# Performance work log

Measured on AMD Instinct MI355X. Metric: run time of the kernel, lower is better.

The kernel has to match this reference:

```python
import jax, jax.numpy as jnp
import numpy as np

# dims
N, E, Z, C, NB = 8192, 131072, 10, 128, 8
R_MAX, P_CUT, AVG_NEIGH = 5.0, 5, 16.0
SH_DIM, N_L, N_LAYERS, MLP_H = 16, 4, 2, 16
# which l each of the 16 sh components belongs to
L_OF_M = jnp.array([0, 1, 1, 1, 2, 2, 2, 2, 2, 3, 3, 3, 3, 3, 3, 3])


def spherical_harmonics(u):
    """Real spherical harmonics up to l=3, e3nn 'component' normalization. u: [E,3] unit vectors."""
    x, y, z = u[:, 0], u[:, 1], u[:, 2]
    x2, y2, z2 = x * x, y * y, z * z
    s3, s5, s15 = np.sqrt(3.0), np.sqrt(5.0), np.sqrt(15.0)
    a33, a32, a31, a30 = 0.25 * np.sqrt(70.0), np.sqrt(105.0), 0.25 * np.sqrt(42.0), 0.5 * np.sqrt(7.0)
    Y = [jnp.ones_like(x),
         s3 * x, s3 * y, s3 * z,
         s15 * x * y, s15 * y * z, 0.5 * s5 * (3 * z2 - 1.0), s15 * x * z, 0.5 * s15 * (x2 - y2),
         a33 * y * (3 * x2 - y2), a32 * x * y * z, a31 * y * (5 * z2 - 1.0),
         a30 * z * (5 * z2 - 3.0), a31 * x * (5 * z2 - 1.0), 0.5 * a32 * z * (x2 - y2),
         a33 * x * (x2 - 3 * y2)]
    return jnp.stack(Y, axis=-1)  # [E,16]


def radial_embedding(r):
    """Bessel radial basis with smooth polynomial cutoff (p=5). r: [E] edge lengths."""
    x = r / R_MAX
    p = float(P_CUT)
    cut = (1.0 - 0.5 * (p + 1.0) * (p + 2.0) * x ** P_CUT
           + p * (p + 2.0) * x ** (P_CUT + 1) - 0.5 * p * (p + 1.0) * x ** (P_CUT + 2))
    cut = jnp.where(x < 1.0, cut, 0.0)
    n = jnp.arange(1, NB + 1, dtype=r.dtype)
    bessel = np.sqrt(2.0 / R_MAX) * jnp.sin(n[None, :] * jnp.pi * x[:, None]) / r[:, None]
    return bessel * cut[:, None]  # [E,8]


def _forward(positions, node_attrs, shifts, W_embed, W_up, R_w1, R_w2, R_w3,
             W_out, w_sc, w_prod, W_plin, w_ro0, ro_w1, ro_w2, edge_index):
    sender, receiver = edge_index[0], edge_index[1]
    vec = positions[receiver] - positions[sender] + shifts          # [E,3]
    lengths = jnp.linalg.norm(vec, axis=-1) + 1e-9                  # [E]
    sh = spherical_harmonics(vec / lengths[:, None])                # [E,16]
    edge_feats = radial_embedding(lengths)                          # [E,8]

    # node embedding: scalars into l=0 slot of [N,C,16]
    scalars = node_attrs @ W_embed                                  # [N,C]
    feats = jnp.zeros((N, C, SH_DIM), scalars.dtype).at[:, :, 0].set(scalars)

    outputs = []
    for L in range(N_LAYERS):
        # linear up (channel mixing, per irrep component)
        h = jnp.einsum('ncm,cd->ndm', feats, W_up[L])               # [N,C,16]
        # radial MLP -> per-edge, per-channel, per-l tensor-product weights
        r = jax.nn.silu(edge_feats @ R_w1[L])
        r = jax.nn.silu(r @ R_w2[L])
        w = (r @ R_w3[L]).reshape(E, C, N_L)                        # [E,C,4]
        w_m = jnp.take(w, L_OF_M, axis=2)                           # [E,C,16]
        # channel-wise tensor product: scalar node feat x SH, scatter to receiver
        msg = h[sender, :, 0][:, :, None] * w_m * sh[:, None, :]    # [E,C,16]
        agg = jax.ops.segment_sum(msg, receiver, num_segments=N) / AVG_NEIGH
        m = jnp.einsum('ncm,cd->ndm', agg, W_out[L])                # [N,C,16]
        # element-dependent skip connection
        sc = h * (node_attrs @ w_sc[L])[:, :, None]
        # product basis (correlation 3): element-weighted powers of scalar part
        s = m[:, :, 0]                                              # [N,C]
        coeff = jnp.einsum('nz,zck->nck', node_attrs, w_prod[L])    # [N,C,3]
        powers = jnp.stack([jnp.ones_like(s), s, s * s], axis=-1)   # [N,C,3]
        scale = jnp.sum(coeff * powers, axis=-1)                    # [N,C]
        feats = jnp.einsum('ncm,cd->ndm', m * scale[:, :, None], W_plin[L]) + sc
        if L == 0:
            outputs.append(feats[:, :, 0] @ w_ro0)                  # linear readout [N]
        else:
            outputs.append(jax.nn.silu(feats[:, :, 0] @ ro_w1) @ ro_w2)  # nonlinear readout [N]
    return outputs[0] + outputs[1]


def setup_inputs() -> dict:
    key = jax.random.key(0)
    ks = jax.random.split(key, 16)
    positions = jax.random.normal(ks[0], (N, 3), jnp.float32) * 1.5
    elems = jax.random.randint(ks[1], (N,), 0, Z)
    node_attrs = jax.nn.one_hot(elems, Z, dtype=jnp.float32)
    edge_index = jax.random.randint(ks[2], (2, E), 0, N)
    shifts = jnp.zeros((E, 3), jnp.float32)
    g = lambda k, sh, fan: jax.random.normal(k, sh, jnp.float32) / np.sqrt(fan)
    return {
        'positions': positions, 'node_attrs': node_attrs, 'shifts': shifts,
        'W_embed': g(ks[3], (Z, C), Z),
        'W_up': g(ks[4], (N_LAYERS, C, C), C),
        'R_w1': g(ks[5], (N_LAYERS, NB, 64), NB),
        'R_w2': g(ks[6], (N_LAYERS, 64, 64), 64),
        'R_w3': g(ks[7], (N_LAYERS, 64, C * N_L), 64),
        'W_out': g(ks[8], (N_LAYERS, C, C), C),
        'w_sc': g(ks[9], (N_LAYERS, Z, C), 1),
        'w_prod': g(ks[10], (N_LAYERS, Z, C, 3), 1) * 0.1,
        'W_plin': g(ks[11], (N_LAYERS, C, C), C),
        'w_ro0': g(ks[12], (C,), C),
        'ro_w1': g(ks[13], (C, MLP_H), C),
        'ro_w2': g(ks[14], (MLP_H,), MLP_H),
        'edge_index': edge_index,
    }


def reference(positions, node_attrs, shifts, W_embed, W_up, R_w1, R_w2, R_w3,
              W_out, w_sc, w_prod, W_plin, w_ro0, ro_w1, ro_w2, edge_index):
    return _forward(positions, node_attrs, shifts, W_embed, W_up, R_w1, R_w2, R_w3,
                    W_out, w_sc, w_prod, W_plin, w_ro0, ro_w1, ro_w2, edge_index)
```

## Files before the change

kernel.cpp:

```cpp
#include <hip/hip_runtime.h>
#include <math.h>

constexpr int kN = 8192;
constexpr int kE = 131072;
constexpr int kHalfN = 4096;
constexpr int kWbTiles = 544;
constexpr int kWbRows  = kWbTiles * 128;

typedef short bf16x8 __attribute__((ext_vector_type(8)));
typedef float f32x4 __attribute__((ext_vector_type(4)));
typedef unsigned short ushort_t;
typedef unsigned int uint_t;

__device__ __forceinline__ float silu_f(float x) { return x / (1.f + __expf(-x)); }

__device__ __forceinline__ ushort_t f2b(float f) {
  uint_t x = __float_as_uint(f);
  uint_t r = (x + 0x7fffu + ((x >> 16) & 1u)) >> 16;
  return (ushort_t)r;
}
__device__ __forceinline__ float b2f(ushort_t u) {
  return __uint_as_float(((uint_t)u) << 16);
}

__global__ __launch_bounds__(256) void zero_ints_kernel(int* __restrict__ a, int* __restrict__ b) {
  int i = blockIdx.x * 256 + threadIdx.x;
  if (i < kN) { a[i] = 0; b[i] = 0; }
}

__global__ __launch_bounds__(256) void elem_kernel(const float* __restrict__ attrs, int* __restrict__ elem) {
  int n = blockIdx.x * 256 + threadIdx.x;
  if (n >= kN) return;
  const float* a = attrs + (size_t)n * 10;
  int best = 0; float bv = a[0];
  #pragma unroll
  for (int z = 1; z < 10; ++z) { float v = a[z]; if (v > bv) { bv = v; best = z; } }
  elem[n] = best;
}

__global__ __launch_bounds__(256) void init_feats_kernel(const float* __restrict__ W_embed,
                                                         const int* __restrict__ elem,
                                                         ushort_t* __restrict__ F) {
  int i = blockIdx.x * 256 + threadIdx.x;
  int n = i >> 7, c = i & 127;
  F[(size_t)n * 2048 + c] = f2b(W_embed[(size_t)elem[n] * 128 + c]);
}

__global__ __launch_bounds__(256) void count_kernel(const int* __restrict__ ei, int* __restrict__ counts) {
  int e = blockIdx.x * 256 + threadIdx.x;
  if (e < kE) atomicAdd(&counts[ei[kE + e]], 1);
}

__global__ __launch_bounds__(1024) void scan_kernel(const int* __restrict__ counts, int* __restrict__ offs) {
  __shared__ int tmp[1024];
  int t = threadIdx.x;
  int loc[8]; int s = 0;
  #pragma unroll
  for (int i = 0; i < 8; ++i) { loc[i] = s; s += counts[t*8 + i]; }
  tmp[t] = s;
  __syncthreads();
  for (int d = 1; d < 1024; d <<= 1) {
    int v = (t >= d) ? tmp[t - d] : 0;
    __syncthreads();
    tmp[t] += v;
    __syncthreads();
  }
  int pre = (t == 0) ? 0 : tmp[t - 1];
  #pragma unroll
  for (int i = 0; i < 8; ++i) offs[t*8 + i] = pre + loc[i];
  if (t == 1023) offs[kN] = tmp[1023];
}

__global__ __launch_bounds__(256) void fill_kernel(const int* __restrict__ ei, const int* __restrict__ offs,
                                                   int* __restrict__ cursor, int* __restrict__ eids,
                                                   int* __restrict__ sends) {
  int e = blockIdx.x * 256 + threadIdx.x;
  if (e >= kE) return;
  int s = ei[e];
  int r = ei[kE + e];
  int pos = atomicAdd(&cursor[r], 1);
  eids[offs[r] + pos] = e;
  sends[offs[r] + pos] = s;
}

__global__ __launch_bounds__(256) void geom_kernel(const float* __restrict__ pos,
                                                   const float* __restrict__ shifts,
                                                   const int* __restrict__ ei,
                                                   const int* __restrict__ eids,
                                                   const int* __restrict__ sends,
                                                   float* __restrict__ sh,
                                                   float* __restrict__ rb) {
  int slot = blockIdx.x * 256 + threadIdx.x;
  if (slot >= kE) return;
  int e = eids[slot];
  int s = sends[slot];
  int r = ei[kE + e];
  float vx = pos[r*3+0] - pos[s*3+0] + shifts[(size_t)e*3+0];
  float vy = pos[r*3+1] - pos[s*3+1] + shifts[(size_t)e*3+1];
  float vz = pos[r*3+2] - pos[s*3+2] + shifts[(size_t)e*3+2];
  float len = sqrtf(vx*vx + vy*vy + vz*vz) + 1e-9f;
  float inv = 1.f / len;
  float x = vx*inv, y = vy*inv, z = vz*inv;
  float x2 = x*x, y2 = y*y, z2 = z*z;
  const float s3  = 1.7320508075688772f;
  const float s5  = 2.2360679774997896f;
  const float s15 = 3.8729833462074170f;
  const float a33 = 2.0916500663351889f;
  const float a32 = 10.246950765959598f;
  const float a31 = 1.6201851746019651f;
  const float a30 = 1.3228756555322954f;
  float4* shp = (float4*)(sh + (size_t)slot * 16);
  shp[0] = make_float4(1.f, s3*x, s3*y, s3*z);
  shp[1] = make_float4(s15*x*y, s15*y*z, 0.5f*s5*(3.f*z2 - 1.f), s15*x*z);
  shp[2] = make_float4(0.5f*s15*(x2 - y2), a33*y*(3.f*x2 - y2), a32*x*y*z, a31*y*(5.f*z2 - 1.f));
  shp[3] = make_float4(a30*z*(5.f*z2 - 3.f), a31*x*(5.f*z2 - 1.f), 0.5f*a32*z*(x2 - y2), a33*x*(x2 - 3.f*y2));
  float xr = len * 0.2f;
  float cut = 0.f;
  if (xr < 1.f) {
    float x5 = xr*xr*xr*xr*xr;
    cut = 1.f - 21.f*x5 + 35.f*x5*xr - 15.f*x5*xr*xr;
  }
  float pref = 0.63245553203367587f * cut * inv;
  const float PI = 3.14159265358979323846f;
  float theta = PI * xr;
  float sn, cs;
  __sincosf(theta, &sn, &cs);
  float twoc = 2.f * cs;
  float b[8];
  float s_prev = 0.f, s_cur = sn;
  b[0] = pref * s_cur;
  #pragma unroll
  for (int k = 1; k < 8; ++k) {
    float s_next = twoc * s_cur - s_prev;
    s_prev = s_cur; s_cur = s_next;
    b[k] = pref * s_cur;
  }
  float4* rbp = (float4*)(rb + (size_t)slot * 8);
  rbp[0] = make_float4(b[0], b[1], b[2], b[3]);
  rbp[1] = make_float4(b[4], b[5], b[6], b[7]);
}

__global__ __launch_bounds__(256) void radial_kernel(const float* __restrict__ rb,
                                                     const float* __restrict__ W1,
                                                     const float* __restrict__ W2,
                                                     ushort_t* __restrict__ r2) {
  __shared__ float rbs[128][8];
  __shared__ float W1s[8*64];
  __shared__ ushort_t B2s[64][72];
  __shared__ ushort_t r1s[128][72];
  const int tid = threadIdx.x;
  const size_t ebase = (size_t)blockIdx.x * 128;
  {
    int r = tid >> 1, q = tid & 1;
    *(float4*)&rbs[r][q*4] = *(const float4*)&rb[(ebase + r)*8 + q*4];
  }
  for (int i = tid; i < 512; i += 256) W1s[i] = W1[i];
  for (int i = tid; i < 4096; i += 256) {
    int k = i >> 6, col = i & 63;
    B2s[col][k] = f2b(W2[i]);
  }
  __syncthreads();
  {
    int col = tid & 63;
    int r0 = (tid >> 6) * 32;
    #pragma unroll 4
    for (int rr = 0; rr < 32; ++rr) {
      int row = r0 + rr;
      float v = 0.f;
      #pragma unroll
      for (int i = 0; i < 8; ++i) v = fmaf(rbs[row][i], W1s[i*64 + col], v);
      r1s[row][col] = f2b(silu_f(v));
    }
  }
  __syncthreads();
  const int lane = tid & 63, wv = tid >> 6;
  const int wr = wv * 32;
  const int fr = lane & 15, kg = (lane >> 4) * 8;
  f32x4 acc[2][4] = {};
  #pragma unroll
  for (int ks = 0; ks < 2; ++ks) {
    const int k0 = ks*32 + kg;
    bf16x8 af[2], bfr[4];
    #pragma unroll
    for (int i = 0; i < 2; ++i) af[i] = *(const bf16x8*)&r1s[wr + i*16 + fr][k0];
    #pragma unroll
    for (int j = 0; j < 4; ++j) bfr[j] = *(const bf16x8*)&B2s[j*16 + fr][k0];
    #pragma unroll
    for (int i = 0; i < 2; ++i)
      #pragma unroll
      for (int j = 0; j < 4; ++j)
        acc[i][j] = __builtin_amdgcn_mfma_f32_16x16x32_bf16(af[i], bfr[j], acc[i][j], 0, 0, 0);
  }
  __syncthreads();
  const int dcol = lane & 15, drow4 = (lane >> 4) * 4;
  #pragma unroll
  for (int i = 0; i < 2; ++i)
    #pragma unroll
    for (int j = 0; j < 4; ++j)
      #pragma unroll
      for (int r = 0; r < 4; ++r) {
        int row = wr + i*16 + drow4 + r;
        int col = j*16 + dcol;
        r1s[row][col] = f2b(silu_f(acc[i][j][r]));
      }
  __syncthreads();
  for (int idx = tid * 8; idx < 128*64; idx += 256*8) {
    int r = idx >> 6, k = idx & 63;
    *(int4*)&r2[(ebase + r)*64 + k] = *(const int4*)&r1s[r][k];
  }
}

__global__ __launch_bounds__(256) void transpose_w_kernel(const float* __restrict__ W, ushort_t* __restrict__ WT) {
  int i = blockIdx.x * 256 + threadIdx.x;
  int d = i >> 7, c = i & 127;
  WT[i] = f2b(W[c*128 + d]);
}

__global__ __launch_bounds__(256) void transpose_r3_kernel(const float* __restrict__ R3, ushort_t* __restrict__ R3T) {
  int i = blockIdx.x * 256 + threadIdx.x;
  int t = i >> 6, j = i & 63;
  int c = t & 127, l = t >> 7;
  R3T[i] = f2b(R3[j*512 + c*4 + l]);
}

template<bool SCALED, bool EPI, bool L0>
__global__ __launch_bounds__(256) void mgemm_kernel(
    const ushort_t* __restrict__ A, size_t aStride,
    const ushort_t* __restrict__ BT,
    ushort_t* __restrict__ O, size_t oStride,
    const float* __restrict__ scaleBuf,
    const ushort_t* __restrict__ Hbuf,
    const float* __restrict__ wscL,
    const int* __restrict__ elem)
{
  __shared__ ushort_t As[128][136];
  __shared__ ushort_t Bs[128][136];
  const int tid = threadIdx.x;
  const size_t rowbase = (size_t)blockIdx.x * 128;

  for (int idx = tid * 8; idx < 128 * 128; idx += 256 * 8) {
    int r = idx >> 7, k = idx & 127;
    *(int4*)&Bs[r][k] = *(const int4*)&BT[(size_t)r * 128 + k];
  }
  for (int idx = tid * 8; idx < 128 * 128; idx += 256 * 8) {
    int r = idx >> 7, k = idx & 127;
    size_t grow = rowbase + r;
    const ushort_t* ap = A + grow * aStride + k;
    if (SCALED) {
      const float* sp = scaleBuf + (grow >> 4) * 128 + k;
      uint_t u[4];
      #pragma unroll
      for (int q = 0; q < 4; ++q) {
        ushort_t lo = f2b(b2f(ap[2*q])   * sp[2*q]);
        ushort_t hi = f2b(b2f(ap[2*q+1]) * sp[2*q+1]);
        u[q] = (uint_t)lo | ((uint_t)hi << 16);
      }
      *(int4*)&As[r][k] = make_int4((int)u[0], (int)u[1], (int)u[2], (int)u[3]);
    } else {
      *(int4*)&As[r][k] = *(const int4*)ap;
    }
  }
  __syncthreads();

  const int lane = tid & 63, wv = tid >> 6;
  const int wr = (wv >> 1) * 64, wc = (wv & 1) * 64;
  const int fr = lane & 15;
  const int kg = (lane >> 4) * 8;
  f32x4 acc[4][4] = {};
  #pragma unroll
  for (int ks = 0; ks < 4; ++ks) {
    const int k0 = ks * 32 + kg;
    bf16x8 af[4], bfr[4];
    #pragma unroll
    for (int i = 0; i < 4; ++i) af[i]  = *(const bf16x8*)&As[wr + i*16 + fr][k0];
    #pragma unroll
    for (int j = 0; j < 4; ++j) bfr[j] = *(const bf16x8*)&Bs[wc + j*16 + fr][k0];
    #pragma unroll
    for (int i = 0; i < 4; ++i)
      #pragma unroll
      for (int j = 0; j < 4; ++j)
        acc[i][j] = __builtin_amdgcn_mfma_f32_16x16x32_bf16(af[i], bfr[j], acc[i][j], 0, 0, 0);
  }

  const int dcol = lane & 15, drow4 = (lane >> 4) * 4;
  #pragma unroll
  for (int i = 0; i < 4; ++i) {
    #pragma unroll
    for (int j = 0; j < 4; ++j) {
      int col = wc + j*16 + dcol;
      #pragma unroll
      for (int r = 0; r < 4; ++r) {
        int row = wr + i*16 + drow4 + r;
        size_t grow = rowbase + row;
        float v = acc[i][j][r];
        if (EPI) {
          if (!L0 || ((grow & 15) == 0)) {
            int ee = elem[grow >> 4];
            v += b2f(Hbuf[grow * 128 + col]) * wscL[(size_t)ee * 128 + col];
          }
        }
        O[grow * oStride + col] = f2b(v);
      }
    }
  }
}

__global__ __launch_bounds__(256) void wgemm_kernel(
    const ushort_t* __restrict__ r2,
    const int* __restrict__ offs, int nb0,
    const ushort_t* __restrict__ R3T, ushort_t* __restrict__ wb)
{
  __shared__ ushort_t As[128][72];
  __shared__ ushort_t Bs[128][72];
  const int tid = threadIdx.x;
  const int rowbase = blockIdx.x * 128;
  const int colbase = blockIdx.y * 128;
  const int halfStart = offs[nb0];

  for (int idx = tid * 8; idx < 128 * 64; idx += 256 * 8) {
    int r = idx >> 6, k = idx & 63;
    *(int4*)&Bs[r][k] = *(const int4*)&R3T[(size_t)(colbase + r) * 64 + k];
  }
  for (int idx = tid * 8; idx < 128 * 64; idx += 256 * 8) {
    int r = idx >> 6, k = idx & 63;
    int slot = halfStart + rowbase + r;
    if (slot > kE - 1) slot = kE - 1;
    *(int4*)&As[r][k] = *(const int4*)&r2[(size_t)slot * 64 + k];
  }
  __syncthreads();

  const int lane = tid & 63, wv = tid >> 6;
  const int wr = (wv >> 1) * 64, wc = (wv & 1) * 64;
  const int fr = lane & 15;
  const int kg = (lane >> 4) * 8;
  f32x4 acc[4][4] = {};
  #pragma unroll
  for (int ks = 0; ks < 2; ++ks) {
    const int k0 = ks * 32 + kg;
    bf16x8 af[4], bfr[4];
    #pragma unroll
    for (int i = 0; i < 4; ++i) af[i]  = *(const bf16x8*)&As[wr + i*16 + fr][k0];
    #pragma unroll
    for (int j = 0; j < 4; ++j) bfr[j] = *(const bf16x8*)&Bs[wc + j*16 + fr][k0];
    #pragma unroll
    for (int i = 0; i < 4; ++i)
      #pragma unroll
      for (int j = 0; j < 4; ++j)
        acc[i][j] = __builtin_amdgcn_mfma_f32_16x16x32_bf16(af[i], bfr[j], acc[i][j], 0, 0, 0);
  }

  const int dcol = lane & 15, drow4 = (lane >> 4) * 4;
  #pragma unroll
  for (int i = 0; i < 4; ++i) {
    #pragma unroll
    for (int j = 0; j < 4; ++j) {
      int col = colbase + wc + j*16 + dcol;
      #pragma unroll
      for (int r = 0; r < 4; ++r) {
        int row = rowbase + wr + i*16 + drow4 + r;
        wb[(size_t)row * 512 + col] = f2b(acc[i][j][r]);
      }
    }
  }
}

constexpr int CH = 32;
__global__ __launch_bounds__(512) void gather_kernel(
    const int* __restrict__ offs, const int* __restrict__ sends, int nb0,
    const ushort_t* __restrict__ wb,
    const float* __restrict__ shcsr,
    const ushort_t* __restrict__ H,
    ushort_t* __restrict__ AGG)
{
  __shared__ ushort_t h0s[CH][136];
  __shared__ float shs[CH][16];
  const int n = nb0 + blockIdx.x;
  const int t = threadIdx.x;
  const int l = t >> 7;
  const int c = t & 127;
  const int wstart = offs[nb0];
  const int e0 = offs[n], e1 = offs[n+1];
  const int mb = l * l;
  const int mc = 2 * l + 1;
  float a[7] = {};
  for (int base = e0; base < e1; base += CH) {
    if (base != e0) __syncthreads();
    uint_t wr[CH];
    #pragma unroll
    for (int j = 0; j < CH; ++j)
      wr[j] = (base + j < e1) ? (uint_t)wb[(size_t)(base - wstart + j) * 512 + t] : 0u;
    {
      int row = t >> 4, seg = t & 15;
      int4 v = make_int4(0, 0, 0, 0);
      if (base + row < e1) v = *(const int4*)&H[(size_t)sends[base + row] * 2048 + seg * 8];
      *(int4*)&h0s[row][seg * 8] = v;
    }
    if (t < 128) {
      int row = t >> 2, seg = t & 3;
      float4 v = make_float4(0.f, 0.f, 0.f, 0.f);
      if (base + row < e1) v = *(const float4*)&shcsr[(size_t)(base + row) * 16 + seg * 4];
      *(float4*)&shs[row][seg * 4] = v;
    }
    __syncthreads();
    #pragma unroll
    for (int j = 0; j < CH; ++j) {
      if (base + j < e1) {
        float wh = b2f((ushort_t)wr[j]) * b2f(h0s[j][c]);
        #pragma unroll
        for (int mi = 0; mi < 7; ++mi)
          if (mi < mc) a[mi] = fmaf(wh, shs[j][mb + mi], a[mi]);
      }
    }
  }
  const float inv16 = 0.0625f;
  #pragma unroll
  for (int mi = 0; mi < 7; ++mi)
    if (mi < mc)
      AGG[(size_t)n * 2048 + (mb + mi) * 128 + c] = f2b(a[mi] * inv16);
}

__global__ __launch_bounds__(256) void scale_kernel(const ushort_t* __restrict__ M,
                                                    const int* __restrict__ elem,
                                                    const float* __restrict__ wprodL,
                                                    float* __restrict__ scale) {
  int i = blockIdx.x * 256 + threadIdx.x;
  int n = i >> 7, c = i & 127;
  float s = b2f(M[(size_t)n * 2048 + c]);
  const float* co = wprodL + ((size_t)elem[n] * 128 + c) * 3;
  scale[i] = co[0] + s * (co[1] + s * co[2]);
}

__global__ __launch_bounds__(64) void readout_kernel(const ushort_t* __restrict__ F,
                                                     const float* __restrict__ ro0,
                                                     const float* __restrict__ ro1,
                                                     const float* __restrict__ ro2,
                                                     float* __restrict__ out, int layer) {
  int n = blockIdx.x; int t = threadIdx.x;
  const ushort_t* fr = F + (size_t)n * 2048;
  float f0 = b2f(fr[t]), f1 = b2f(fr[t + 64]);
  if (layer == 0) {
    float v = f0 * ro0[t] + f1 * ro0[t + 64];
    #pragma unroll
    for (int m = 32; m > 0; m >>= 1) v += __shfl_xor(v, m, 64);
    if (t == 0) out[n] = v;
  } else {
    float acc = 0.f;
    for (int h = 0; h < 16; ++h) {
      float p = f0 * ro1[t*16 + h] + f1 * ro1[(t + 64)*16 + h];
      #pragma unroll
      for (int m = 32; m > 0; m >>= 1) p += __shfl_xor(p, m, 64);
      acc = fmaf(silu_f(p), ro2[h], acc);
    }
    if (t == 0) out[n] += acc;
  }
}

extern "C" void kernel_launch(void* const* d_in, const int* in_sizes, int n_in,
                              void* d_out, int out_size, void* d_ws, size_t ws_size,
                              hipStream_t stream) {
  (void)in_sizes; (void)n_in; (void)out_size;
  const float* positions = (const float*)d_in[0];
  const float* node_attrs= (const float*)d_in[1];
  const float* shifts    = (const float*)d_in[2];
  const float* W_embed   = (const float*)d_in[3];
  const float* W_up      = (const float*)d_in[4];
  const float* R_w1      = (const float*)d_in[5];
  const float* R_w2      = (const float*)d_in[6];
  const float* R_w3      = (const float*)d_in[7];
  const float* W_out     = (const float*)d_in[8];
  const float* w_sc      = (const float*)d_in[9];
  const float* w_prod    = (const float*)d_in[10];
  const float* W_plin    = (const float*)d_in[11];
  const float* w_ro0     = (const float*)d_in[12];
  const float* ro_w1     = (const float*)d_in[13];
  const float* ro_w2     = (const float*)d_in[14];
  const int*   ei        = (const int*)d_in[15];
  float* out = (float*)d_out;

  char* ws_ptr = (char*)d_ws;
  size_t off = 0;
  auto alloc = [&](size_t nbytes) -> void* {
    void* p = ws_ptr + off;
    off += (nbytes + 255) & ~(size_t)255;
    return p;
  };
  const size_t PB = (size_t)kN * 16 * 128 * sizeof(ushort_t);
  ushort_t* P0    = (ushort_t*)alloc(PB);
  ushort_t* P1    = (ushort_t*)alloc(PB);
  ushort_t* P2    = (ushort_t*)alloc(PB);
  float* shcsr    = (float*)alloc((size_t)kE * 16 * 4);
  float* rbcsr    = (float*)alloc((size_t)kE * 8 * 4);
  ushort_t* r2csr = (ushort_t*)alloc((size_t)kE * 64 * 2);
  float* scaleb   = (float*)alloc((size_t)kN * 128 * 4);
  ushort_t* wb    = (ushort_t*)alloc((size_t)kWbRows * 512 * 2);
  ushort_t* R3T0  = (ushort_t*)alloc(512 * 64 * 2);
  ushort_t* R3T1  = (ushort_t*)alloc(512 * 64 * 2);
  ushort_t* WTu0  = (ushort_t*)alloc(128 * 128 * 2);
  ushort_t* WTu1  = (ushort_t*)alloc(128 * 128 * 2);
  ushort_t* WTo0  = (ushort_t*)alloc(128 * 128 * 2);
  ushort_t* WTo1  = (ushort_t*)alloc(128 * 128 * 2);
  ushort_t* WTp0  = (ushort_t*)alloc(128 * 128 * 2);
  ushort_t* WTp1  = (ushort_t*)alloc(128 * 128 * 2);
  int* elemb  = (int*)alloc(kN * 4);
  int* counts = (int*)alloc(kN * 4);
  int* cursor = (int*)alloc(kN * 4);
  int* offsb  = (int*)alloc((kN + 1) * 4);
  int* eidsb  = (int*)alloc((size_t)kE * 4);
  int* sendsb = (int*)alloc((size_t)kE * 4);
  if (off > ws_size) return;

  zero_ints_kernel<<<kN/256, 256, 0, stream>>>(counts, cursor);
  elem_kernel<<<kN/256, 256, 0, stream>>>(node_attrs, elemb);
  init_feats_kernel<<<(kN*128)/256, 256, 0, stream>>>(W_embed, elemb, P0);
  count_kernel<<<kE/256, 256, 0, stream>>>(ei, counts);
  scan_kernel<<<1, 1024, 0, stream>>>(counts, offsb);
  fill_kernel<<<kE/256, 256, 0, stream>>>(ei, offsb, cursor, eidsb, sendsb);
  geom_kernel<<<kE/256, 256, 0, stream>>>(positions, shifts, ei, eidsb, sendsb, shcsr, rbcsr);
  transpose_w_kernel<<<64, 256, 0, stream>>>(W_up, WTu0);
  transpose_w_kernel<<<64, 256, 0, stream>>>(W_up + 16384, WTu1);
  transpose_w_kernel<<<64, 256, 0, stream>>>(W_out, WTo0);
  transpose_w_kernel<<<64, 256, 0, stream>>>(W_out + 16384, WTo1);
  transpose_w_kernel<<<64, 256, 0, stream>>>(W_plin, WTp0);
  transpose_w_kernel<<<64, 256, 0, stream>>>(W_plin + 16384, WTp1);
  transpose_r3_kernel<<<128, 256, 0, stream>>>(R_w3, R3T0);
  transpose_r3_kernel<<<128, 256, 0, stream>>>(R_w3 + 32768, R3T1);

  radial_kernel<<<kE/128, 256, 0, stream>>>(rbcsr, R_w1, R_w2, r2csr);
  mgemm_kernel<false,false,false><<<kN/128, 256, 0, stream>>>(
      P0, 2048, WTu0, P1, 2048, nullptr, nullptr, nullptr, nullptr);
  wgemm_kernel<<<dim3(kWbTiles,4), 256, 0, stream>>>(r2csr, offsb, 0, R3T0, wb);
  gather_kernel<<<kHalfN, 512, 0, stream>>>(offsb, sendsb, 0, wb, shcsr, P1, P2);
  wgemm_kernel<<<dim3(kWbTiles,4), 256, 0, stream>>>(r2csr, offsb, kHalfN, R3T0, wb);
  gather_kernel<<<kHalfN, 512, 0, stream>>>(offsb, sendsb, kHalfN, wb, shcsr, P1, P2);
  mgemm_kernel<false,false,false><<<(kN*16)/128, 256, 0, stream>>>(
      P2, 128, WTo0, P0, 128, nullptr, nullptr, nullptr, nullptr);
  scale_kernel<<<(kN*128)/256, 256, 0, stream>>>(P0, elemb, w_prod, scaleb);
  mgemm_kernel<true,true,true><<<(kN*16)/128, 256, 0, stream>>>(
      P0, 128, WTp0, P2, 128, scaleb, P1, w_sc, elemb);
  readout_kernel<<<kN, 64, 0, stream>>>(P2, w_ro0, ro_w1, ro_w2, out, 0);

  radial_kernel<<<kE/128, 256, 0, stream>>>(rbcsr, R_w1 + 512, R_w2 + 4096, r2csr);
  mgemm_kernel<false,false,false><<<(kN*16)/128, 256, 0, stream>>>(
      P2, 128, WTu1, P1, 128, nullptr, nullptr, nullptr, nullptr);
  wgemm_kernel<<<dim3(kWbTiles,4), 256, 0, stream>>>(r2csr, offsb, 0, R3T1, wb);
  gather_kernel<<<kHalfN, 512, 0, stream>>>(offsb, sendsb, 0, wb, shcsr, P1, P0);
  wgemm_kernel<<<dim3(kWbTiles,4), 256, 0, stream>>>(r2csr, offsb, kHalfN, R3T1, wb);
  gather_kernel<<<kHalfN, 512, 0, stream>>>(offsb, sendsb, kHalfN, wb, shcsr, P1, P0);
  mgemm_kernel<false,false,false><<<(kN*16)/128, 256, 0, stream>>>(
      P0, 128, WTo1, P2, 128, nullptr, nullptr, nullptr, nullptr);
  scale_kernel<<<(kN*128)/256, 256, 0, stream>>>(P2, elemb, w_prod + 3840, scaleb);
  mgemm_kernel<true,true,false><<<(kN*16)/128, 256, 0, stream>>>(
      P2, 128, WTp1, P0, 128, scaleb, P1, w_sc + 1280, elemb);
  readout_kernel<<<kN, 64, 0, stream>>>(P0, w_ro0, ro_w1, ro_w2, out, 1);
}
```

Baseline: 568.8 us.

## Fuse sender feature multiply into radial weight GEMM epilogue, simplify gather

```diff
diff --git a/kernel.cpp b/kernel.cpp
--- a/kernel.cpp
+++ b/kernel.cpp
@@ -308,7 +308,9 @@
 __global__ __launch_bounds__(256) void wgemm_kernel(
     const ushort_t* __restrict__ r2,
     const int* __restrict__ offs, int nb0,
-    const ushort_t* __restrict__ R3T, ushort_t* __restrict__ wb)
+    const int* __restrict__ sends,
+    const ushort_t* __restrict__ H,
+    const ushort_t* __restrict__ R3T, ushort_t* __restrict__ whb)
 {
   __shared__ ushort_t As[128][72];
   __shared__ ushort_t Bs[128][72];
@@ -350,69 +352,74 @@
   }
 
   const int dcol = lane & 15, drow4 = (lane >> 4) * 4;
+  int sendv[4][4];
+  #pragma unroll
+  for (int i = 0; i < 4; ++i)
+    #pragma unroll
+    for (int r = 0; r < 4; ++r) {
+      int slot = halfStart + rowbase + wr + i*16 + drow4 + r;
+      if (slot > kE - 1) slot = kE - 1;
+      sendv[i][r] = sends[slot];
+    }
   #pragma unroll
   for (int i = 0; i < 4; ++i) {
     #pragma unroll
     for (int j = 0; j < 4; ++j) {
       int col = colbase + wc + j*16 + dcol;
+      int cc = col & 127;
       #pragma unroll
       for (int r = 0; r < 4; ++r) {
         int row = rowbase + wr + i*16 + drow4 + r;
-        wb[(size_t)row * 512 + col] = f2b(acc[i][j][r]);
+        float h0 = b2f(H[(size_t)sendv[i][r] * 2048 + cc]);
+        whb[(size_t)row * 512 + col] = f2b(acc[i][j][r] * h0);
       }
     }
   }
 }
 
-constexpr int CH = 32;
+constexpr int CH = 16;
 __global__ __launch_bounds__(512) void gather_kernel(
-    const int* __restrict__ offs, const int* __restrict__ sends, int nb0,
-    const ushort_t* __restrict__ wb,
+    const int* __restrict__ offs, int nb0,
+    const ushort_t* __restrict__ whb,
     const float* __restrict__ shcsr,
-    const ushort_t* __restrict__ H,
     ushort_t* __restrict__ AGG)
 {
-  __shared__ ushort_t h0s[CH][136];
+  __shared__ ushort_t ws[CH][512];
   __shared__ float shs[CH][16];
   const int n = nb0 + blockIdx.x;
   const int t = threadIdx.x;
   const int l = t >> 7;
-  const int c = t & 127;
+  const int mb = l * l;
+  const int mc = 2 * l + 1;
   const int wstart = offs[nb0];
   const int e0 = offs[n], e1 = offs[n+1];
-  const int mb = l * l;
-  const int mc = 2 * l + 1;
   float a[7] = {};
   for (int base = e0; base < e1; base += CH) {
-    if (base != e0) __syncthreads();
-    uint_t wr[CH];
-    #pragma unroll
-    for (int j = 0; j < CH; ++j)
-      wr[j] = (base + j < e1) ? (uint_t)wb[(size_t)(base - wstart + j) * 512 + t] : 0u;
-    {
-      int row = t >> 4, seg = t & 15;
-      int4 v = make_int4(0, 0, 0, 0);
-      if (base + row < e1) v = *(const int4*)&H[(size_t)sends[base + row] * 2048 + seg * 8];
-      *(int4*)&h0s[row][seg * 8] = v;
-    }
-    if (t < 128) {
+    const int cnt = min(CH, e1 - base);
+    #pragma unroll
+    for (int rep = 0; rep < 2; ++rep) {
+      int idx = rep * 512 + t;
+      int row = idx >> 6, seg = idx & 63;
+      if (row < cnt)
+        *(int4*)&ws[row][seg * 8] = *(const int4*)&whb[(size_t)(base - wstart + row) * 512 + seg * 8];
+    }
+    if (t < 64) {
       int row = t >> 2, seg = t & 3;
       float4 v = make_float4(0.f, 0.f, 0.f, 0.f);
-      if (base + row < e1) v = *(const float4*)&shcsr[(size_t)(base + row) * 16 + seg * 4];
+      if (row < cnt) v = *(const float4*)&shcsr[(size_t)(base + row) * 16 + seg * 4];
       *(float4*)&shs[row][seg * 4] = v;
     }
     __syncthreads();
-    #pragma unroll
-    for (int j = 0; j < CH; ++j) {
-      if (base + j < e1) {
-        float wh = b2f((ushort_t)wr[j]) * b2f(h0s[j][c]);
-        #pragma unroll
-        for (int mi = 0; mi < 7; ++mi)
-          if (mi < mc) a[mi] = fmaf(wh, shs[j][mb + mi], a[mi]);
-      }
-    }
+    for (int j = 0; j < cnt; ++j) {
+      float whv = b2f(ws[j][t]);
+      #pragma unroll
+      for (int mi = 0; mi < 7; ++mi)
+        if (mi < mc) a[mi] = fmaf(whv, shs[j][mb + mi], a[mi]);
+    }
+    __syncthreads();
   }
   const float inv16 = 0.0625f;
+  const int c = t & 127;
   #pragma unroll
   for (int mi = 0; mi < 7; ++mi)
     if (mi < mc)
@@ -492,7 +499,7 @@
   float* rbcsr    = (float*)alloc((size_t)kE * 8 * 4);
   ushort_t* r2csr = (ushort_t*)alloc((size_t)kE * 64 * 2);
   float* scaleb   = (float*)alloc((size_t)kN * 128 * 4);
-  ushort_t* wb    = (ushort_t*)alloc((size_t)kWbRows * 512 * 2);
+  ushort_t* whb   = (ushort_t*)alloc((size_t)kWbRows * 512 * 2);
   ushort_t* R3T0  = (ushort_t*)alloc(512 * 64 * 2);
   ushort_t* R3T1  = (ushort_t*)alloc(512 * 64 * 2);
   ushort_t* WTu0  = (ushort_t*)alloc(128 * 128 * 2);
@@ -528,10 +535,10 @@
   radial_kernel<<<kE/128, 256, 0, stream>>>(rbcsr, R_w1, R_w2, r2csr);
   mgemm_kernel<false,false,false><<<kN/128, 256, 0, stream>>>(
       P0, 2048, WTu0, P1, 2048, nullptr, nullptr, nullptr, nullptr);
-  wgemm_kernel<<<dim3(kWbTiles,4), 256, 0, stream>>>(r2csr, offsb, 0, R3T0, wb);
-  gather_kernel<<<kHalfN, 512, 0, stream>>>(offsb, sendsb, 0, wb, shcsr, P1, P2);
-  wgemm_kernel<<<dim3(kWbTiles,4), 256, 0, stream>>>(r2csr, offsb, kHalfN, R3T0, wb);
-  gather_kernel<<<kHalfN, 512, 0, stream>>>(offsb, sendsb, kHalfN, wb, shcsr, P1, P2);
+  wgemm_kernel<<<dim3(kWbTiles,4), 256, 0, stream>>>(r2csr, offsb, 0, sendsb, P1, R3T0, whb);
+  gather_kernel<<<kHalfN, 512, 0, stream>>>(offsb, 0, whb, shcsr, P2);
+  wgemm_kernel<<<dim3(kWbTiles,4), 256, 0, stream>>>(r2csr, offsb, kHalfN, sendsb, P1, R3T0, whb);
+  gather_kernel<<<kHalfN, 512, 0, stream>>>(offsb, kHalfN, whb, shcsr, P2);
   mgemm_kernel<false,false,false><<<(kN*16)/128, 256, 0, stream>>>(
       P2, 128, WTo0, P0, 128, nullptr, nullptr, nullptr, nullptr);
   scale_kernel<<<(kN*128)/256, 256, 0, stream>>>(P0, elemb, w_prod, scaleb);
@@ -542,10 +549,10 @@
   radial_kernel<<<kE/128, 256, 0, stream>>>(rbcsr, R_w1 + 512, R_w2 + 4096, r2csr);
   mgemm_kernel<false,false,false><<<(kN*16)/128, 256, 0, stream>>>(
       P2, 128, WTu1, P1, 128, nullptr, nullptr, nullptr, nullptr);
-  wgemm_kernel<<<dim3(kWbTiles,4), 256, 0, stream>>>(r2csr, offsb, 0, R3T1, wb);
-  gather_kernel<<<kHalfN, 512, 0, stream>>>(offsb, sendsb, 0, wb, shcsr, P1, P0);
-  wgemm_kernel<<<dim3(kWbTiles,4), 256, 0, stream>>>(r2csr, offsb, kHalfN, R3T1, wb);
-  gather_kernel<<<kHalfN, 512, 0, stream>>>(offsb, sendsb, kHalfN, wb, shcsr, P1, P0);
+  wgemm_kernel<<<dim3(kWbTiles,4), 256, 0, stream>>>(r2csr, offsb, 0, sendsb, P1, R3T1, whb);
+  gather_kernel<<<kHalfN, 512, 0, stream>>>(offsb, 0, whb, shcsr, P0);
+  wgemm_kernel<<<dim3(kWbTiles,4), 256, 0, stream>>>(r2csr, offsb, kHalfN, sendsb, P1, R3T1, whb);
+  gather_kernel<<<kHalfN, 512, 0, stream>>>(offsb, kHalfN, whb, shcsr, P0);
   mgemm_kernel<false,false,false><<<(kN*16)/128, 256, 0, stream>>>(
       P0, 128, WTo1, P2, 128, nullptr, nullptr, nullptr, nullptr);
   scale_kernel<<<(kN*128)/256, 256, 0, stream>>>(P2, elemb, w_prod + 3840, scaleb);
```

New measurement: 585.3 us. 2.9% more time.
